# Optimization experiments

Measured on AMD Instinct MI355X. Metric: run time of the kernel, lower is better.

## Reference

```python
import jax, jax.numpy as jnp
import numpy as np

B, S, D = 4, 2048, 512
H, DH = 8, 64          # heads, dim_head; inner_dim = H*DH = D
QN, QP = -128, 127     # signed 8-bit range (LSQ, all_positive=False)
UQP = 255              # unsigned 8-bit range for softmax output

# scale-vector layout (one learnable LSQ scale per quantizer, as in the module)
# 0:s_hs 1:s_a_q 2:s_w_q 3:s_a_k 4:s_w_k 5:s_a_v 6:s_w_v
# 7:s_qk_a 8:s_qk_b 9:s_softmax 10:s_av_a 11:s_av_b 12:s_a_out 13:s_w_out

def fq(x, s, qn=QN, qp=QP):
    """LSQ fake quantization: clamp(round(x/s), qn, qp) * s, STE on round."""
    v = jnp.clip(x / s, qn, qp)
    vq = v + jax.lax.stop_gradient(jnp.round(v) - v)
    return vq * s


def setup_inputs() -> dict:
    key = jax.random.key(0)
    ks = jax.random.split(key, 6)
    hs = jax.random.normal(ks[0], (B, S, D), dtype=jnp.float32)
    w_std = 0.02
    Wq = jax.random.normal(ks[1], (D, D), dtype=jnp.float32) * w_std
    Wk = jax.random.normal(ks[2], (D, D), dtype=jnp.float32) * w_std
    Wv = jax.random.normal(ks[3], (D, D), dtype=jnp.float32) * w_std
    Wo = jax.random.normal(ks[4], (D, D), dtype=jnp.float32) * w_std
    bo = jnp.zeros((D,), dtype=jnp.float32)
    scales = jnp.array([
        0.03,    # s_hs: hs ~ N(0,1), clip at ~4 sigma
        0.03, 0.001,   # to_q act / weight
        0.03, 0.001,   # to_k act / weight
        0.03, 0.001,   # to_v act / weight
        0.02, 0.02,    # mul_qk a/b
        1.0 / 255.0,   # softmax output (unsigned)
        1.0 / 255.0, 0.02,  # mul_av a/b
        0.01, 0.001,   # to_out act / weight
    ], dtype=jnp.float32)
    return {"hs": hs, "Wq": Wq, "Wk": Wk, "Wv": Wv, "Wo": Wo, "bo": bo,
            "scales": scales}


def reference(hs, Wq, Wk, Wv, Wo, bo, scales):
    sc = scales
    scale = DH ** (-0.5)
    # quan_hs_before_attn (encoder_hidden_states = hs in self-attention)
    hs_q = fq(hs, sc[0])
    # Linear_Quan: LSQ-quantized activation @ LSQ-quantized weight
    def qlin(x, W, sa, sw):
        return jnp.einsum('bsd,ed->bse', fq(x, sa), fq(W, sw))
    q = qlin(hs_q, Wq, sc[1], sc[2])
    k = qlin(hs_q, Wk, sc[3], sc[4])
    v = qlin(hs_q, Wv, sc[5], sc[6])
    # 'b s (h d) -> b h s d'
    q = q.reshape(B, S, H, DH).transpose(0, 2, 1, 3)
    k = k.reshape(B, S, H, DH).transpose(0, 2, 1, 3)
    v = v.reshape(B, S, H, DH).transpose(0, 2, 1, 3)
    # QuanMMHead(q, k^T): quantize both operands, then matmul
    attn = jnp.einsum('bhsd,bhtd->bhst', fq(q, sc[7]), fq(k, sc[8])) * scale
    # QuanSoftmax: softmax then unsigned 8-bit fake quant of probabilities
    attn = fq(jax.nn.softmax(attn, axis=-1), sc[9], 0, UQP)
    # QuanMMHead(attn, v)
    out = jnp.einsum('bhst,bhtd->bhsd', fq(attn, sc[10]), fq(v, sc[11]))
    # '(b h) s d -> b s (h d)'
    out = out.transpose(0, 2, 1, 3).reshape(B, S, H * DH)
    # to_out[0]: Linear_Quan with bias (dropout is identity in eval)
    out = jnp.einsum('bsd,ed->bse', fq(out, sc[12]), fq(Wo, sc[13])) + bo
    return out
```

## Files before the change

### kernel.cpp

```cpp
#include <hip/hip_runtime.h>

typedef _Float16 half8  __attribute__((ext_vector_type(8)));
typedef float    f32x4  __attribute__((ext_vector_type(4)));
typedef unsigned short ushort8 __attribute__((ext_vector_type(8)));

__device__ __forceinline__ float clampf(float v, float lo, float hi){
    return fminf(fmaxf(v, lo), hi);
}
__device__ __forceinline__ float b2f(unsigned short u){
    unsigned int x = ((unsigned int)u) << 16;
    return __builtin_bit_cast(float, x);
}
__device__ __forceinline__ unsigned short f2b(float f){
    unsigned int u = __builtin_bit_cast(unsigned int, f);
    u += 0x7FFFu + ((u >> 16) & 1u);
    return (unsigned short)(u >> 16);
}
__device__ __forceinline__ float fexp2(float x){ return __builtin_amdgcn_exp2f(x); }

__device__ __forceinline__ void gld_lds16(const _Float16* g, _Float16* lds_uniform){
    __builtin_amdgcn_global_load_lds(
        (const __attribute__((address_space(1))) void*)g,
        (__attribute__((address_space(3))) void*)lds_uniform, 16, 0, 0);
}

#define EW_WALL 0u
#define EW_WO   786432u
#define EW_AQ   1048576u
#define EW_AK   (EW_AQ + 4194304u)
#define EW_AV   (EW_AK + 4194304u)
#define EW_Q    (EW_AV + 4194304u)
#define EW_K    (EW_Q  + 4194304u)
#define EW_VT   (EW_K  + 4194304u)
#define EW_O    (EW_VT + 4194304u)

__global__ __launch_bounds__(256) void k_quant(
    const unsigned short* __restrict__ hs,
    const unsigned short* __restrict__ Wq, const unsigned short* __restrict__ Wk,
    const unsigned short* __restrict__ Wv, const unsigned short* __restrict__ Wo,
    _Float16* __restrict__ w_all, _Float16* __restrict__ wo16,
    _Float16* __restrict__ aq, _Float16* __restrict__ ak, _Float16* __restrict__ av,
    const unsigned short* __restrict__ scu)
{
    int blk = blockIdx.x;
    if (blk < 512){
        int gid  = blk * 256 + threadIdx.x;
        int idx8 = gid * 8;
        int which = idx8 >> 18;
        int rem   = idx8 & 262143;
        const unsigned short* W = (which==0)? Wq : (which==1)? Wk : (which==2)? Wv : Wo;
        float sw = b2f((which<3) ? scu[2 + 2*which] : scu[13]);
        ushort8 w = *(const ushort8*)(W + rem);
        half8 o;
        #pragma unroll
        for (int j=0;j<8;j++)
            o[j] = (_Float16)rintf(clampf(b2f(w[j])/sw, -128.f, 127.f));
        _Float16* dst = (which<3) ? (w_all + which*262144 + rem) : (wo16 + rem);
        *(half8*)dst = o;
    } else {
        int gid = (blk - 512) * 256 + threadIdx.x;
        int i8 = gid * 8;
        float s0 = b2f(scu[0]), s1 = b2f(scu[1]), s3 = b2f(scu[3]), s5 = b2f(scu[5]);
        ushort8 h = *(const ushort8*)(hs + i8);
        half8 q, k, v;
        #pragma unroll
        for (int j=0;j<8;j++){
            float h1 = rintf(clampf(b2f(h[j])/s0, -128.f, 127.f)) * s0;
            q[j] = (_Float16)rintf(clampf(h1/s1, -128.f, 127.f));
            k[j] = (_Float16)rintf(clampf(h1/s3, -128.f, 127.f));
            v[j] = (_Float16)rintf(clampf(h1/s5, -128.f, 127.f));
        }
        *(half8*)(aq+i8) = q;
        *(half8*)(ak+i8) = k;
        *(half8*)(av+i8) = v;
    }
}

__global__ __launch_bounds__(256) void k_gemm_qkv(
    const _Float16* __restrict__ aq, const _Float16* __restrict__ ak,
    const _Float16* __restrict__ av, const _Float16* __restrict__ w_all,
    _Float16* __restrict__ q16, _Float16* __restrict__ k16, _Float16* __restrict__ vt16,
    const unsigned short* __restrict__ scu)
{
    __shared__ __align__(16) union SMem {
        struct { _Float16 At[128][64]; _Float16 Bt[64][64]; } ab;
        _Float16 Vt[64][132];
    } sm;
    int tid = threadIdx.x;
    int m0 = blockIdx.x*128, n0 = blockIdx.y*64;
    int proj = blockIdx.y >> 3;
    const _Float16* Ag = (proj==0)? aq : (proj==1)? ak : av;
    int w = tid>>6, lane = tid&63, l15 = lane&15, quad = lane>>4;
    int wm = w>>1, wn = w&1;
    f32x4 z = {0.f,0.f,0.f,0.f};
    f32x4 acc[4][2];
    #pragma unroll
    for (int i=0;i<4;i++)
      #pragma unroll
      for (int j=0;j<2;j++) acc[i][j] = z;

    for (int k0=0; k0<512; k0+=64){
        #pragma unroll
        for (int it=0; it<4; it++){
            int idx = it*256 + tid;
            int row = idx>>3, col = (idx&7)*8;
            int ubase = (it*256 + w*64)*8;
            gld_lds16(Ag + (m0+row)*512 + k0 + col, &sm.ab.At[0][0] + ubase);
        }
        #pragma unroll
        for (int it=0; it<2; it++){
            int idx = it*256 + tid;
            int row = idx>>3, col = (idx&7)*8;
            int ubase = (it*256 + w*64)*8;
            gld_lds16(w_all + (n0+row)*512 + k0 + col, &sm.ab.Bt[0][0] + ubase);
        }
        __syncthreads();
        half8 af[4][2], bf[2][2];
        #pragma unroll
        for (int mt=0; mt<4; mt++){
            af[mt][0] = *(const half8*)(&sm.ab.At[wm*64+mt*16+l15][quad*8]);
            af[mt][1] = *(const half8*)(&sm.ab.At[wm*64+mt*16+l15][32+quad*8]);
        }
        #pragma unroll
        for (int nt=0; nt<2; nt++){
            bf[nt][0] = *(const half8*)(&sm.ab.Bt[wn*32+nt*16+l15][quad*8]);
            bf[nt][1] = *(const half8*)(&sm.ab.Bt[wn*32+nt*16+l15][32+quad*8]);
        }
        #pragma unroll
        for (int mt=0; mt<4; mt++)
          #pragma unroll
          for (int nt=0; nt<2; nt++){
            acc[mt][nt] = __builtin_amdgcn_mfma_f32_16x16x32_f16(af[mt][0], bf[nt][0], acc[mt][nt], 0,0,0);
            acc[mt][nt] = __builtin_amdgcn_mfma_f32_16x16x32_f16(af[mt][1], bf[nt][1], acc[mt][nt], 0,0,0);
          }
        __syncthreads();
    }

    float ssc = b2f(scu[1+2*proj]) * b2f(scu[2+2*proj]);
    float qs  = b2f((proj==0)? scu[7] : (proj==1)? scu[8] : scu[11]);
    if (proj < 2){
        #pragma unroll
        for (int mt=0; mt<4; mt++){
          #pragma unroll
          for (int nt=0; nt<2; nt++){
            int n = n0 + wn*32 + nt*16 + l15;
            int nloc = n & 511;
            int h = nloc>>6, d = nloc&63;
            #pragma unroll
            for (int r=0;r<4;r++){
              int m = m0 + wm*64 + mt*16 + quad*4 + r;
              int b = m>>11, s = m&2047;
              int bh = b*8 + h;
              float val = acc[mt][nt][r] * ssc;
              float qv = rintf(clampf(val/qs, -128.f, 127.f));
              if (proj==0) q16[(bh*2048 + s)*64 + d] = (_Float16)qv;
              else         k16[(bh*2048 + s)*64 + d] = (_Float16)qv;
            }
          }
        }
    } else {
        #pragma unroll
        for (int mt=0; mt<4; mt++){
          #pragma unroll
          for (int nt=0; nt<2; nt++){
            int nl = wn*32 + nt*16 + l15;
            #pragma unroll
            for (int r=0;r<4;r++){
              int ml = wm*64 + mt*16 + quad*4 + r;
              float val = acc[mt][nt][r] * ssc;
              sm.Vt[nl][ml] = (_Float16)rintf(clampf(val/qs, -128.f, 127.f));
            }
          }
        }
        __syncthreads();
        int vrow = tid >> 2;
        int vcol = (tid & 3) * 32;
        int nloc2 = (n0 & 511) + vrow;
        int h2 = nloc2 >> 6, d2 = nloc2 & 63;
        int bh2 = (m0 >> 11)*8 + h2;
        int s2 = (m0 & 2047) + vcol;
        _Float16* dst = vt16 + (bh2*64 + d2)*2048 + s2;
        #pragma unroll
        for (int i=0;i<4;i++)
            *(half8*)(dst + i*8) = *(const half8*)(&sm.Vt[vrow][vcol + i*8]);
    }
}

__global__ __launch_bounds__(512, 4) void k_attn(
    const _Float16* __restrict__ q16, const _Float16* __restrict__ k16,
    const _Float16* __restrict__ vt16, _Float16* __restrict__ o16,
    const unsigned short* __restrict__ scu)
{
    __shared__ __align__(16) _Float16 Kbuf[2][64][72];
    __shared__ __align__(16) _Float16 p16[8][16][72];
    int tid = threadIdx.x;
    int w = tid>>6, lane = tid&63, l15 = lane&15, quad = lane>>4;
    int bh = blockIdx.x;
    int q0 = blockIdx.y*128 + w*16;
    float s9 = b2f(scu[9]), s10 = b2f(scu[10]);
    float al2 = b2f(scu[7]) * b2f(scu[8]) * 0.125f * 1.44269504088896341f;

    f32x4 z = {0.f,0.f,0.f,0.f};
    const _Float16* qr = q16 + (bh*2048 + q0 + l15)*64;
    half8 aq0 = *(const half8*)(qr + quad*8);
    half8 aq1 = *(const half8*)(qr + 32 + quad*8);

    const _Float16* kg    = k16  + bh*131072;
    const _Float16* vbase = vt16 + bh*131072;
    int srow = tid>>3, scol = (tid&7)*8;

    half8 kst = *(const half8*)(kg + tid*8);

    float l[4] = {0.f, 0.f, 0.f, 0.f};
    float cmx[32];

    #pragma unroll
    for (int ch=0; ch<32; ch++){
        int buf = ch & 1;
        *(half8*)(&Kbuf[buf][srow][scol]) = kst;
        __syncthreads();
        if (ch < 31)
            kst = *(const half8*)(kg + (ch+1)*4096 + tid*8);
        f32x4 s[4];
        #pragma unroll
        for (int j=0;j<4;j++){
            half8 bk0 = *(const half8*)(&Kbuf[buf][j*16+l15][quad*8]);
            half8 bk1 = *(const half8*)(&Kbuf[buf][j*16+l15][32+quad*8]);
            f32x4 t = __builtin_amdgcn_mfma_f32_16x16x32_f16(aq0, bk0, z, 0,0,0);
            s[j]    = __builtin_amdgcn_mfma_f32_16x16x32_f16(aq1, bk1, t, 0,0,0);
        }
        float mj[4];
        #pragma unroll
        for (int j=0;j<4;j++){
            mj[j] = fmaxf(fmaxf(s[j][0], s[j][1]), fmaxf(s[j][2], s[j][3]));
            #pragma unroll
            for (int r=0;r<4;r++)
                l[r] += fexp2(s[j][r]*al2);
        }
        cmx[ch] = fmaxf(fmaxf(mj[0], mj[1]), fmaxf(mj[2], mj[3]));
    }

    #pragma unroll
    for (int r=0;r<4;r++){
        #pragma unroll
        for (int d=1; d<16; d<<=1)
            l[r] += __shfl_xor(l[r], d, 64);
    }
    float inv_s9 = 1.0f / s9;
    float r910   = s9 / s10;
    float lq9[4];
    #pragma unroll
    for (int r=0;r<4;r++) lq9[r] = log2f(inv_s9 / l[r]);
    float lml = fmaxf(fmaxf(lq9[0], lq9[1]), fmaxf(lq9[2], lq9[3]));
    unsigned int mask = 0u;
    #pragma unroll
    for (int ch=0; ch<32; ch++){
        if (__ballot(fmaf(cmx[ch], al2, lml) > -1.0001f)) mask |= (1u << ch);
    }

    f32x4 oacc[4];
    #pragma unroll
    for (int dt=0; dt<4; dt++) oacc[dt] = z;
    for (int ch=0; ch<32; ch++){
        if (!(mask & (1u << ch))) continue;
        const _Float16* kc = kg + ch*4096;
        f32x4 s[4];
        #pragma unroll
        for (int j=0;j<4;j++){
            const _Float16* kr = kc + (j*16+l15)*64;
            half8 bk0 = *(const half8*)(kr + quad*8);
            half8 bk1 = *(const half8*)(kr + 32 + quad*8);
            f32x4 t = __builtin_amdgcn_mfma_f32_16x16x32_f16(aq0, bk0, z, 0,0,0);
            s[j]    = __builtin_amdgcn_mfma_f32_16x16x32_f16(aq1, bk1, t, 0,0,0);
        }
        float rmax[4];
        #pragma unroll
        for (int r=0;r<4;r++)
            rmax[r] = fmaxf(fmaxf(s[0][r], s[1][r]), fmaxf(s[2][r], s[3][r]));
        float rb = fmaxf(fmaxf(fmaf(rmax[0], al2, lq9[0]), fmaf(rmax[1], al2, lq9[1])),
                         fmaxf(fmaf(rmax[2], al2, lq9[2]), fmaf(rmax[3], al2, lq9[3])));
        if (!__ballot(rb > -1.0001f)) continue;

        float av[4][4];
        float amax = 0.f;
        #pragma unroll
        for (int j=0;j<4;j++){
            #pragma unroll
            for (int r=0;r<4;r++){
                float p1i = rintf(fminf(fexp2(fmaf(s[j][r], al2, lq9[r])), 255.f));
                float a   = rintf(fminf(p1i*r910, 127.f));
                av[j][r] = a;
                amax = fmaxf(amax, a);
            }
        }
        if (__ballot(amax > 0.f)){
            #pragma unroll
            for (int j=0;j<4;j++)
                #pragma unroll
                for (int r=0;r<4;r++)
                    p16[w][quad*4+r][j*16+l15] = (_Float16)av[j][r];
            half8 ap0 = *(const half8*)(&p16[w][l15][quad*8]);
            half8 ap1 = *(const half8*)(&p16[w][l15][32+quad*8]);
            #pragma unroll
            for (int dt=0; dt<4; dt++){
                const _Float16* vr0 = vbase + (dt*16+l15)*2048 + ch*64;
                half8 b0 = *(const half8*)(vr0 + quad*8);
                half8 b1 = *(const half8*)(vr0 + 32 + quad*8);
                oacc[dt] = __builtin_amdgcn_mfma_f32_16x16x32_f16(ap0, b0, oacc[dt], 0,0,0);
                oacc[dt] = __builtin_amdgcn_mfma_f32_16x16x32_f16(ap1, b1, oacc[dt], 0,0,0);
            }
        }
    }

    float s1011 = b2f(scu[10]) * b2f(scu[11]);
    float s12   = b2f(scu[12]);
    int b = bh>>3, h = bh&7;
    #pragma unroll
    for (int dt=0; dt<4; dt++){
        #pragma unroll
        for (int r=0;r<4;r++){
            float o = oacc[dt][r] * s1011;
            _Float16 v = (_Float16)rintf(clampf(o/s12, -128.f, 127.f));
            o16[(b*2048 + q0 + quad*4 + r)*512 + h*64 + dt*16 + l15] = v;
        }
    }
}

__global__ __launch_bounds__(256) void k_gemm_out(
    const _Float16* __restrict__ o16, const _Float16* __restrict__ wo16,
    const unsigned short* __restrict__ bo, unsigned short* __restrict__ out,
    const unsigned short* __restrict__ scu)
{
    __shared__ __align__(16) _Float16 At[64][64];
    __shared__ __align__(16) _Float16 Bt[64][64];
    int tid = threadIdx.x;
    int m0 = blockIdx.x*64, n0 = blockIdx.y*64;
    int w = tid>>6, lane = tid&63, l15 = lane&15, quad = lane>>4;
    int wm = w>>1, wn = w&1;
    f32x4 z = {0.f,0.f,0.f,0.f};
    f32x4 acc[2][2];
    #pragma unroll
    for (int i=0;i<2;i++)
      #pragma unroll
      for (int j=0;j<2;j++) acc[i][j] = z;

    for (int k0=0; k0<512; k0+=64){
        #pragma unroll
        for (int it=0; it<2; it++){
            int idx = it*256 + tid;
            int row = idx>>3, col = (idx&7)*8;
            int ubase = (it*256 + w*64)*8;
            gld_lds16(o16  + (m0+row)*512 + k0 + col, &At[0][0] + ubase);
        }
        #pragma unroll
        for (int it=0; it<2; it++){
            int idx = it*256 + tid;
            int row = idx>>3, col = (idx&7)*8;
            int ubase = (it*256 + w*64)*8;
            gld_lds16(wo16 + (n0+row)*512 + k0 + col, &Bt[0][0] + ubase);
        }
        __syncthreads();
        half8 af[2][2], bf[2][2];
        #pragma unroll
        for (int mt=0; mt<2; mt++){
            af[mt][0] = *(const half8*)(&At[wm*32+mt*16+l15][quad*8]);
            af[mt][1] = *(const half8*)(&At[wm*32+mt*16+l15][32+quad*8]);
        }
        #pragma unroll
        for (int nt=0; nt<2; nt++){
            bf[nt][0] = *(const half8*)(&Bt[wn*32+nt*16+l15][quad*8]);
            bf[nt][1] = *(const half8*)(&Bt[wn*32+nt*16+l15][32+quad*8]);
        }
        #pragma unroll
        for (int mt=0; mt<2; mt++)
          #pragma unroll
          for (int nt=0; nt<2; nt++){
            acc[mt][nt] = __builtin_amdgcn_mfma_f32_16x16x32_f16(af[mt][0], bf[nt][0], acc[mt][nt], 0,0,0);
            acc[mt][nt] = __builtin_amdgcn_mfma_f32_16x16x32_f16(af[mt][1], bf[nt][1], acc[mt][nt], 0,0,0);
          }
        __syncthreads();
    }

    float ssc = b2f(scu[12]) * b2f(scu[13]);
    #pragma unroll
    for (int mt=0; mt<2; mt++){
      #pragma unroll
      for (int nt=0; nt<2; nt++){
        int n = n0 + wn*32 + nt*16 + l15;
        float bn = b2f(bo[n]);
        #pragma unroll
        for (int r=0;r<4;r++){
          int m = m0 + wm*32 + mt*16 + quad*4 + r;
          out[m*512 + n] = f2b(acc[mt][nt][r]*ssc + bn);
        }
      }
    }
}

extern "C" void kernel_launch(void* const* d_in, const int* in_sizes, int n_in,
                              void* d_out, int out_size, void* d_ws, size_t ws_size,
                              hipStream_t stream)
{
    const unsigned short* hs = (const unsigned short*)d_in[0];
    const unsigned short* Wq = (const unsigned short*)d_in[1];
    const unsigned short* Wk = (const unsigned short*)d_in[2];
    const unsigned short* Wv = (const unsigned short*)d_in[3];
    const unsigned short* Wo = (const unsigned short*)d_in[4];
    const unsigned short* bo = (const unsigned short*)d_in[5];
    const unsigned short* sc = (const unsigned short*)d_in[6];
    unsigned short* out = (unsigned short*)d_out;

    _Float16* wsh   = (_Float16*)d_ws;
    _Float16* w_all = wsh + EW_WALL;
    _Float16* wo16  = wsh + EW_WO;
    _Float16* a_q   = wsh + EW_AQ;
    _Float16* a_k   = wsh + EW_AK;
    _Float16* a_v   = wsh + EW_AV;
    _Float16* q16   = wsh + EW_Q;
    _Float16* k16   = wsh + EW_K;
    _Float16* vt16  = wsh + EW_VT;
    _Float16* o16   = wsh + EW_O;

    k_quant<<<2560, 256, 0, stream>>>(hs, Wq, Wk, Wv, Wo, w_all, wo16,
                                      a_q, a_k, a_v, sc);
    k_gemm_qkv<<<dim3(64,24), 256, 0, stream>>>(a_q, a_k, a_v, w_all, q16, k16, vt16, sc);
    k_attn<<<dim3(32,16), 512, 0, stream>>>(q16, k16, vt16, o16, sc);
    k_gemm_out<<<dim3(128,8), 256, 0, stream>>>(o16, wo16, bo, out, sc);
}
```

Measured before the change: 154.2 us.

## Switch QKV and output projections to int8 storage and int8 MFMA

Quantized activations and weights are stored as signed int8 instead of fp16 integer values, and the QKV and output GEMMs use the 16x16x64 i8 MFMA with int32 accumulation. This halves the intermediate traffic for the quantized activations and weights and doubles the K per MFMA instruction. The attention kernel now writes int8 output. Integer accumulation is exact for these clamped ranges, so results should match. LDS tile load indexing is rewritten for 16-byte int8 chunks.

```diff
diff --git a/kernel.cpp b/kernel.cpp
--- a/kernel.cpp
+++ b/kernel.cpp
@@ -2,7 +2,9 @@
 
 typedef _Float16 half8  __attribute__((ext_vector_type(8)));
 typedef float    f32x4  __attribute__((ext_vector_type(4)));
+typedef int      i32x4  __attribute__((ext_vector_type(4)));
 typedef unsigned short ushort8 __attribute__((ext_vector_type(8)));
+typedef signed char char8 __attribute__((ext_vector_type(8)));
 
 __device__ __forceinline__ float clampf(float v, float lo, float hi){
     return fminf(fmaxf(v, lo), hi);
@@ -18,28 +20,29 @@
 }
 __device__ __forceinline__ float fexp2(float x){ return __builtin_amdgcn_exp2f(x); }
 
-__device__ __forceinline__ void gld_lds16(const _Float16* g, _Float16* lds_uniform){
+__device__ __forceinline__ void gld_lds16(const void* g, void* lds_uniform){
     __builtin_amdgcn_global_load_lds(
         (const __attribute__((address_space(1))) void*)g,
         (__attribute__((address_space(3))) void*)lds_uniform, 16, 0, 0);
 }
 
-#define EW_WALL 0u
-#define EW_WO   786432u
-#define EW_AQ   1048576u
-#define EW_AK   (EW_AQ + 4194304u)
-#define EW_AV   (EW_AK + 4194304u)
-#define EW_Q    (EW_AV + 4194304u)
-#define EW_K    (EW_Q  + 4194304u)
-#define EW_VT   (EW_K  + 4194304u)
-#define EW_O    (EW_VT + 4194304u)
+#define BW_WALL 0u
+#define BW_WO   786432u
+#define BW_AQ   1048576u
+#define BW_AK   (BW_AQ + 4194304u)
+#define BW_AV   (BW_AK + 4194304u)
+#define BW_Q    (BW_AV + 4194304u)
+#define BW_K    (BW_Q  + 8388608u)
+#define BW_VT   (BW_K  + 8388608u)
+#define BW_O    (BW_VT + 8388608u)
 
 __global__ __launch_bounds__(256) void k_quant(
     const unsigned short* __restrict__ hs,
     const unsigned short* __restrict__ Wq, const unsigned short* __restrict__ Wk,
     const unsigned short* __restrict__ Wv, const unsigned short* __restrict__ Wo,
-    _Float16* __restrict__ w_all, _Float16* __restrict__ wo16,
-    _Float16* __restrict__ aq, _Float16* __restrict__ ak, _Float16* __restrict__ av,
+    signed char* __restrict__ w_all, signed char* __restrict__ wo8,
+    signed char* __restrict__ aq, signed char* __restrict__ ak,
+    signed char* __restrict__ av,
     const unsigned short* __restrict__ scu)
 {
     int blk = blockIdx.x;
@@ -51,49 +54,49 @@
         const unsigned short* W = (which==0)? Wq : (which==1)? Wk : (which==2)? Wv : Wo;
         float sw = b2f((which<3) ? scu[2 + 2*which] : scu[13]);
         ushort8 w = *(const ushort8*)(W + rem);
-        half8 o;
+        char8 o;
         #pragma unroll
         for (int j=0;j<8;j++)
-            o[j] = (_Float16)rintf(clampf(b2f(w[j])/sw, -128.f, 127.f));
-        _Float16* dst = (which<3) ? (w_all + which*262144 + rem) : (wo16 + rem);
-        *(half8*)dst = o;
+            o[j] = (signed char)rintf(clampf(b2f(w[j])/sw, -128.f, 127.f));
+        signed char* dst = (which<3) ? (w_all + which*262144 + rem) : (wo8 + rem);
+        *(char8*)dst = o;
     } else {
         int gid = (blk - 512) * 256 + threadIdx.x;
         int i8 = gid * 8;
         float s0 = b2f(scu[0]), s1 = b2f(scu[1]), s3 = b2f(scu[3]), s5 = b2f(scu[5]);
         ushort8 h = *(const ushort8*)(hs + i8);
-        half8 q, k, v;
+        char8 q, k, v;
         #pragma unroll
         for (int j=0;j<8;j++){
             float h1 = rintf(clampf(b2f(h[j])/s0, -128.f, 127.f)) * s0;
-            q[j] = (_Float16)rintf(clampf(h1/s1, -128.f, 127.f));
-            k[j] = (_Float16)rintf(clampf(h1/s3, -128.f, 127.f));
-            v[j] = (_Float16)rintf(clampf(h1/s5, -128.f, 127.f));
-        }
-        *(half8*)(aq+i8) = q;
-        *(half8*)(ak+i8) = k;
-        *(half8*)(av+i8) = v;
+            q[j] = (signed char)rintf(clampf(h1/s1, -128.f, 127.f));
+            k[j] = (signed char)rintf(clampf(h1/s3, -128.f, 127.f));
+            v[j] = (signed char)rintf(clampf(h1/s5, -128.f, 127.f));
+        }
+        *(char8*)(aq+i8) = q;
+        *(char8*)(ak+i8) = k;
+        *(char8*)(av+i8) = v;
     }
 }
 
 __global__ __launch_bounds__(256) void k_gemm_qkv(
-    const _Float16* __restrict__ aq, const _Float16* __restrict__ ak,
-    const _Float16* __restrict__ av, const _Float16* __restrict__ w_all,
+    const signed char* __restrict__ aq, const signed char* __restrict__ ak,
+    const signed char* __restrict__ av, const signed char* __restrict__ w_all,
     _Float16* __restrict__ q16, _Float16* __restrict__ k16, _Float16* __restrict__ vt16,
     const unsigned short* __restrict__ scu)
 {
     __shared__ __align__(16) union SMem {
-        struct { _Float16 At[128][64]; _Float16 Bt[64][64]; } ab;
+        struct { signed char At[128][64]; signed char Bt[64][64]; } ab;
         _Float16 Vt[64][132];
     } sm;
     int tid = threadIdx.x;
     int m0 = blockIdx.x*128, n0 = blockIdx.y*64;
     int proj = blockIdx.y >> 3;
-    const _Float16* Ag = (proj==0)? aq : (proj==1)? ak : av;
+    const signed char* Ag = (proj==0)? aq : (proj==1)? ak : av;
     int w = tid>>6, lane = tid&63, l15 = lane&15, quad = lane>>4;
     int wm = w>>1, wn = w&1;
-    f32x4 z = {0.f,0.f,0.f,0.f};
-    f32x4 acc[4][2];
+    i32x4 z = {0,0,0,0};
+    i32x4 acc[4][2];
     #pragma unroll
     for (int i=0;i<4;i++)
       #pragma unroll
@@ -101,38 +104,30 @@
 
     for (int k0=0; k0<512; k0+=64){
         #pragma unroll
-        for (int it=0; it<4; it++){
-            int idx = it*256 + tid;
-            int row = idx>>3, col = (idx&7)*8;
-            int ubase = (it*256 + w*64)*8;
-            gld_lds16(Ag + (m0+row)*512 + k0 + col, &sm.ab.At[0][0] + ubase);
-        }
-        #pragma unroll
         for (int it=0; it<2; it++){
             int idx = it*256 + tid;
-            int row = idx>>3, col = (idx&7)*8;
-            int ubase = (it*256 + w*64)*8;
+            int row = idx>>2, col = (idx&3)*16;
+            int ubase = (it*256 + w*64)*16;
+            gld_lds16(Ag + (m0+row)*512 + k0 + col, &sm.ab.At[0][0] + ubase);
+        }
+        {
+            int row = tid>>2, col = (tid&3)*16;
+            int ubase = (w*64)*16;
             gld_lds16(w_all + (n0+row)*512 + k0 + col, &sm.ab.Bt[0][0] + ubase);
         }
         __syncthreads();
-        half8 af[4][2], bf[2][2];
-        #pragma unroll
-        for (int mt=0; mt<4; mt++){
-            af[mt][0] = *(const half8*)(&sm.ab.At[wm*64+mt*16+l15][quad*8]);
-            af[mt][1] = *(const half8*)(&sm.ab.At[wm*64+mt*16+l15][32+quad*8]);
-        }
-        #pragma unroll
-        for (int nt=0; nt<2; nt++){
-            bf[nt][0] = *(const half8*)(&sm.ab.Bt[wn*32+nt*16+l15][quad*8]);
-            bf[nt][1] = *(const half8*)(&sm.ab.Bt[wn*32+nt*16+l15][32+quad*8]);
-        }
+        i32x4 af[4], bf[2];
+        #pragma unroll
+        for (int mt=0; mt<4; mt++)
+            af[mt] = *(const i32x4*)(&sm.ab.At[wm*64+mt*16+l15][quad*16]);
+        #pragma unroll
+        for (int nt=0; nt<2; nt++)
+            bf[nt] = *(const i32x4*)(&sm.ab.Bt[wn*32+nt*16+l15][quad*16]);
         #pragma unroll
         for (int mt=0; mt<4; mt++)
           #pragma unroll
-          for (int nt=0; nt<2; nt++){
-            acc[mt][nt] = __builtin_amdgcn_mfma_f32_16x16x32_f16(af[mt][0], bf[nt][0], acc[mt][nt], 0,0,0);
-            acc[mt][nt] = __builtin_amdgcn_mfma_f32_16x16x32_f16(af[mt][1], bf[nt][1], acc[mt][nt], 0,0,0);
-          }
+          for (int nt=0; nt<2; nt++)
+            acc[mt][nt] = __builtin_amdgcn_mfma_i32_16x16x64_i8(af[mt], bf[nt], acc[mt][nt], 0,0,0);
         __syncthreads();
     }
 
@@ -151,7 +146,7 @@
               int m = m0 + wm*64 + mt*16 + quad*4 + r;
               int b = m>>11, s = m&2047;
               int bh = b*8 + h;
-              float val = acc[mt][nt][r] * ssc;
+              float val = (float)acc[mt][nt][r] * ssc;
               float qv = rintf(clampf(val/qs, -128.f, 127.f));
               if (proj==0) q16[(bh*2048 + s)*64 + d] = (_Float16)qv;
               else         k16[(bh*2048 + s)*64 + d] = (_Float16)qv;
@@ -167,7 +162,7 @@
             #pragma unroll
             for (int r=0;r<4;r++){
               int ml = wm*64 + mt*16 + quad*4 + r;
-              float val = acc[mt][nt][r] * ssc;
+              float val = (float)acc[mt][nt][r] * ssc;
               sm.Vt[nl][ml] = (_Float16)rintf(clampf(val/qs, -128.f, 127.f));
             }
           }
@@ -188,7 +183,7 @@
 
 __global__ __launch_bounds__(512, 4) void k_attn(
     const _Float16* __restrict__ q16, const _Float16* __restrict__ k16,
-    const _Float16* __restrict__ vt16, _Float16* __restrict__ o16,
+    const _Float16* __restrict__ vt16, signed char* __restrict__ o8,
     const unsigned short* __restrict__ scu)
 {
     __shared__ __align__(16) _Float16 Kbuf[2][64][72];
@@ -320,64 +315,54 @@
         #pragma unroll
         for (int r=0;r<4;r++){
             float o = oacc[dt][r] * s1011;
-            _Float16 v = (_Float16)rintf(clampf(o/s12, -128.f, 127.f));
-            o16[(b*2048 + q0 + quad*4 + r)*512 + h*64 + dt*16 + l15] = v;
+            signed char v = (signed char)rintf(clampf(o/s12, -128.f, 127.f));
+            o8[(b*2048 + q0 + quad*4 + r)*512 + h*64 + dt*16 + l15] = v;
         }
     }
 }
 
 __global__ __launch_bounds__(256) void k_gemm_out(
-    const _Float16* __restrict__ o16, const _Float16* __restrict__ wo16,
+    const signed char* __restrict__ o8, const signed char* __restrict__ wo8,
     const unsigned short* __restrict__ bo, unsigned short* __restrict__ out,
     const unsigned short* __restrict__ scu)
 {
-    __shared__ __align__(16) _Float16 At[64][64];
-    __shared__ __align__(16) _Float16 Bt[64][64];
+    __shared__ __align__(16) signed char At[64][64];
+    __shared__ __align__(16) signed char Bt[64][64];
     int tid = threadIdx.x;
     int m0 = blockIdx.x*64, n0 = blockIdx.y*64;
     int w = tid>>6, lane = tid&63, l15 = lane&15, quad = lane>>4;
     int wm = w>>1, wn = w&1;
-    f32x4 z = {0.f,0.f,0.f,0.f};
-    f32x4 acc[2][2];
+    i32x4 z = {0,0,0,0};
+    i32x4 acc[2][2];
     #pragma unroll
     for (int i=0;i<2;i++)
       #pragma unroll
       for (int j=0;j<2;j++) acc[i][j] = z;
 
     for (int k0=0; k0<512; k0+=64){
-        #pragma unroll
-        for (int it=0; it<2; it++){
-            int idx = it*256 + tid;
-            int row = idx>>3, col = (idx&7)*8;
-            int ubase = (it*256 + w*64)*8;
-            gld_lds16(o16  + (m0+row)*512 + k0 + col, &At[0][0] + ubase);
-        }
-        #pragma unroll
-        for (int it=0; it<2; it++){
-            int idx = it*256 + tid;
-            int row = idx>>3, col = (idx&7)*8;
-            int ubase = (it*256 + w*64)*8;
-            gld_lds16(wo16 + (n0+row)*512 + k0 + col, &Bt[0][0] + ubase);
-        }
-        __syncthreads();
-        half8 af[2][2], bf[2][2];
-        #pragma unroll
-        for (int mt=0; mt<2; mt++){
-            af[mt][0] = *(const half8*)(&At[wm*32+mt*16+l15][quad*8]);
-            af[mt][1] = *(const half8*)(&At[wm*32+mt*16+l15][32+quad*8]);
-        }
-        #pragma unroll
-        for (int nt=0; nt<2; nt++){
-            bf[nt][0] = *(const half8*)(&Bt[wn*32+nt*16+l15][quad*8]);
-            bf[nt][1] = *(const half8*)(&Bt[wn*32+nt*16+l15][32+quad*8]);
-        }
+        {
+            int row = tid>>2, col = (tid&3)*16;
+            int ubase = (w*64)*16;
+            gld_lds16(o8  + (m0+row)*512 + k0 + col, &At[0][0] + ubase);
+        }
+        {
+            int row = tid>>2, col = (tid&3)*16;
+            int ubase = (w*64)*16;
+            gld_lds16(wo8 + (n0+row)*512 + k0 + col, &Bt[0][0] + ubase);
+        }
+        __syncthreads();
+        i32x4 af[2], bf[2];
+        #pragma unroll
+        for (int mt=0; mt<2; mt++)
+            af[mt] = *(const i32x4*)(&At[wm*32+mt*16+l15][quad*16]);
+        #pragma unroll
+        for (int nt=0; nt<2; nt++)
+            bf[nt] = *(const i32x4*)(&Bt[wn*32+nt*16+l15][quad*16]);
         #pragma unroll
         for (int mt=0; mt<2; mt++)
           #pragma unroll
-          for (int nt=0; nt<2; nt++){
-            acc[mt][nt] = __builtin_amdgcn_mfma_f32_16x16x32_f16(af[mt][0], bf[nt][0], acc[mt][nt], 0,0,0);
-            acc[mt][nt] = __builtin_amdgcn_mfma_f32_16x16x32_f16(af[mt][1], bf[nt][1], acc[mt][nt], 0,0,0);
-          }
+          for (int nt=0; nt<2; nt++)
+            acc[mt][nt] = __builtin_amdgcn_mfma_i32_16x16x64_i8(af[mt], bf[nt], acc[mt][nt], 0,0,0);
         __syncthreads();
     }
 
@@ -391,7 +376,7 @@
         #pragma unroll
         for (int r=0;r<4;r++){
           int m = m0 + wm*32 + mt*16 + quad*4 + r;
-          out[m*512 + n] = f2b(acc[mt][nt][r]*ssc + bn);
+          out[m*512 + n] = f2b((float)acc[mt][nt][r]*ssc + bn);
         }
       }
     }
@@ -410,20 +395,20 @@
     const unsigned short* sc = (const unsigned short*)d_in[6];
     unsigned short* out = (unsigned short*)d_out;
 
-    _Float16* wsh   = (_Float16*)d_ws;
-    _Float16* w_all = wsh + EW_WALL;
-    _Float16* wo16  = wsh + EW_WO;
-    _Float16* a_q   = wsh + EW_AQ;
-    _Float16* a_k   = wsh + EW_AK;
-    _Float16* a_v   = wsh + EW_AV;
-    _Float16* q16   = wsh + EW_Q;
-    _Float16* k16   = wsh + EW_K;
-    _Float16* vt16  = wsh + EW_VT;
-    _Float16* o16   = wsh + EW_O;
-
-    k_quant<<<2560, 256, 0, stream>>>(hs, Wq, Wk, Wv, Wo, w_all, wo16,
+    unsigned char* ws = (unsigned char*)d_ws;
+    signed char* w_all = (signed char*)(ws + BW_WALL);
+    signed char* wo8   = (signed char*)(ws + BW_WO);
+    signed char* a_q   = (signed char*)(ws + BW_AQ);
+    signed char* a_k   = (signed char*)(ws + BW_AK);
+    signed char* a_v   = (signed char*)(ws + BW_AV);
+    _Float16*    q16   = (_Float16*)(ws + BW_Q);
+    _Float16*    k16   = (_Float16*)(ws + BW_K);
+    _Float16*    vt16  = (_Float16*)(ws + BW_VT);
+    signed char* o8    = (signed char*)(ws + BW_O);
+
+    k_quant<<<2560, 256, 0, stream>>>(hs, Wq, Wk, Wv, Wo, w_all, wo8,
                                       a_q, a_k, a_v, sc);
     k_gemm_qkv<<<dim3(64,24), 256, 0, stream>>>(a_q, a_k, a_v, w_all, q16, k16, vt16, sc);
-    k_attn<<<dim3(32,16), 512, 0, stream>>>(q16, k16, vt16, o16, sc);
-    k_gemm_out<<<dim3(128,8), 256, 0, stream>>>(o16, wo16, bo, out, sc);
-}
+    k_attn<<<dim3(32,16), 512, 0, stream>>>(q16, k16, vt16, o8, sc);
+    k_gemm_out<<<dim3(128,8), 256, 0, stream>>>(o8, wo8, bo, out, sc);
+}
```

After: 144.5 us. 1.07x faster.
